# Kernel optimization log

Measured on AMD Instinct MI355X. Metric: run time of the kernel, lower is better.

The kernel has to match this reference:

```python
import jax, jax.numpy as jnp
import numpy as np
import math

# ---- hyperparameters (from __init__) ----
S = 64.0
M = 0.45
EASY_MARGIN = False
ALPHA = 0.0
BETA = 0.0
EPS_OT = 0.1   # self.eps
NITER = 6      # self.niter
COS_M = math.cos(M)
SIN_M = math.sin(M)
TH = math.cos(math.pi - M)
MM = math.sin(math.pi - M) * M

# ---- shapes ----
B = 24
D_EMB = 512
N_CLASSES = 10000
C_CH = 256   # channels -> number of OT points per image
H = 14       # spatial -> point dim H*H = 196


def setup_inputs() -> dict:
    key = jax.random.key(0)
    k1, k2, k3, k4 = jax.random.split(key, 4)
    embeddings = jax.random.normal(k1, (B, D_EMB), dtype=jnp.float32)
    conv_features = jax.random.normal(k2, (B, C_CH, H, H), dtype=jnp.float32)
    label = jax.random.randint(k3, (B,), 0, 8)
    # nn.init.normal_(kernel, std=0.01)
    kernel = jax.random.normal(k4, (D_EMB, N_CLASSES), dtype=jnp.float32) * 0.01
    return {"embeddings": embeddings, "conv_features": conv_features,
            "kernel": kernel, "label": label, "epoch": 1}


def _cdist(x, y):
    # Euclidean pairwise distance via GEMM: x (n,d), y (m,d) -> (n,m)
    x2 = jnp.sum(x * x, axis=-1)[:, None]
    y2 = jnp.sum(y * y, axis=-1)[None, :]
    d2 = jnp.maximum(x2 + y2 - 2.0 * (x @ y.T), 0.0)
    return jnp.sqrt(d2 + 1e-12)


def _sinkhorn_dist(x, y):
    # Entropic OT distance <T, C> with uniform marginals, log-domain Sinkhorn.
    C = _cdist(x, y)                       # (n, m)
    n, m = C.shape
    log_mu = -jnp.log(jnp.float32(n))
    log_nu = -jnp.log(jnp.float32(m))
    f = jnp.zeros((n,), C.dtype)
    g = jnp.zeros((m,), C.dtype)
    for _ in range(NITER):  # fixed 6 iterations
        f = -EPS_OT * jax.nn.logsumexp((g[None, :] - C) / EPS_OT + log_nu, axis=1)
        g = -EPS_OT * jax.nn.logsumexp((f[:, None] - C) / EPS_OT + log_mu, axis=0)
    T = jnp.exp((f[:, None] + g[None, :] - C) / EPS_OT + log_mu + log_nu)
    return jnp.sum(T * C)


def reference(embeddings, conv_features, kernel, label, epoch):
    b = embeddings.shape[0]
    emb = embeddings / jnp.linalg.norm(embeddings, axis=1, keepdims=True)
    kn = kernel / jnp.linalg.norm(kernel, axis=0, keepdims=True)
    cos_theta = jnp.clip(emb @ kn, -1.0, 1.0)          # (B, n_classes)
    origin_cos = cos_theta

    rows = jnp.arange(b)
    tl = cos_theta[rows, label]                         # target logit (B,)
    sin_t = jnp.sqrt(jnp.maximum(1.0 - tl * tl, 0.0))
    ctm = tl * COS_M - sin_t * SIN_M
    if EASY_MARGIN:
        ftl = jnp.where(tl > 0.0, ctm, tl)
    else:
        ftl = jnp.where(tl > TH, ctm, tl - MM)
    cos_theta = cos_theta.at[rows, label].set(ftl)
    arcfaceloss = cos_theta * S

    # ---- triplet mining on embedding cosine similarities ----
    dists = emb @ emb.T                                 # (B, B) cosine sims
    eq = label[:, None] == label[None, :]               # (B, B) same-class mask
    # diff_low[a,p,n] = cos(a,n) - cos(a,p)
    diff = dists[:, None, :] - dists[:, :, None]        # (a, p, n)
    valid = eq[:, :, None] & (~eq)[:, None, :] & (diff > -ALPHA)
    n_cosine_pair = jnp.sum(valid)

    if epoch >= 0:
        feats = conv_features.reshape(b, conv_features.shape[1], -1)  # (B, C, H*H)
        # batched Sinkhorn distance for all (a,b) image pairs: (B, B)
        D = jax.vmap(lambda xa: jax.vmap(lambda xb: _sinkhorn_dist(xa, xb))(feats))(feats)
        dis = jnp.maximum(D[:, :, None] - D[:, None, :], -BETA)       # (a, p, n)
        hit = valid & (dis > 0.0)
        ot_pair = jnp.sum(hit)
        wass = jnp.sum(jnp.where(hit, dis, 0.0))
        wass_loss = jnp.where(wass > 0.0,
                              wass / jnp.maximum(ot_pair, 1).astype(wass.dtype),
                              jnp.zeros((), wass.dtype))
    else:
        ot_pair = jnp.zeros((), jnp.int32)
        wass_loss = jnp.zeros(())

    return (arcfaceloss, wass_loss, origin_cos * S, n_cosine_pair, ot_pair)
```

## Files before the change

### kernel.cpp

```cpp
#include <hip/hip_runtime.h>
#include <math.h>

#define B_SZ 24
#define D_EMBD 512
#define N_CLS 10000
#define CC 256
#define HH 196

#define S_SCALE 64.0f
#define COS_M 0.9004471023526769f
#define SIN_M 0.43496553411123023f
#define TH_C (-0.9004471023526769f)
#define MM_C 0.19573449035005357f
#define KSC 14.4269504088896f
#define C2E 0.0693147180559945f

typedef short bfrag8 __attribute__((ext_vector_type(8)));
typedef float facc4 __attribute__((ext_vector_type(4)));

#if __has_builtin(__builtin_amdgcn_exp2f)
#define EXP2F(x) __builtin_amdgcn_exp2f(x)
#else
#define EXP2F(x) exp2f(x)
#endif
#if __has_builtin(__builtin_amdgcn_logf)
#define LOG2F(x) __builtin_amdgcn_logf(x)
#else
#define LOG2F(x) __log2f(x)
#endif

__device__ inline unsigned short f2bf_rne(float x) {
    union { float f; unsigned u; } cv; cv.f = x;
    unsigned r = cv.u + 0x7FFFu + ((cv.u >> 16) & 1u);
    return (unsigned short)(r >> 16);
}
__device__ inline float bf2f(unsigned short h) {
    union { unsigned u; float f; } cv; cv.u = ((unsigned)h) << 16; return cv.f;
}

__global__ __launch_bounds__(1024) void k_pairs_all(const float* __restrict__ emb,
        const float* __restrict__ conv, float* __restrict__ dists,
        float* __restrict__ Dmat) {
    const int t = threadIdx.x;
    const int bid = blockIdx.x;

    if (bid >= 276) {
        int l = t & 63, w16 = t >> 6;
        if (bid == 276 && t < B_SZ) Dmat[t * B_SZ + t] = 0.f;
        int pid = (bid - 276) * 16 + w16;
        if (pid >= B_SZ * B_SZ) return;
        int i = pid / B_SZ, j = pid - (pid / B_SZ) * B_SZ;
        float sij = 0.f, sii = 0.f, sjj = 0.f;
        #pragma unroll
        for (int u = 0; u < 8; ++u) {
            float vi = emb[i*D_EMBD + u*64 + l];
            float vj = emb[j*D_EMBD + u*64 + l];
            sij = fmaf(vi, vj, sij); sii = fmaf(vi, vi, sii); sjj = fmaf(vj, vj, sjj);
        }
        #pragma unroll
        for (int o = 1; o < 64; o <<= 1) {
            sij += __shfl_xor(sij, o, 64);
            sii += __shfl_xor(sii, o, 64);
            sjj += __shfl_xor(sjj, o, 64);
        }
        if (l == 0) dists[pid] = sij * rsqrtf(sii * sjj);
        return;
    }

    __shared__ __align__(16) char smem[65536];
    unsigned short* Ah = (unsigned short*)smem;
    unsigned short* Al = Ah + 8192;
    unsigned short* Bh = Al + 8192;
    unsigned short* Bl = Bh + 8192;
    float* rowred = (float*)smem;
    float* colred = rowred + 1024;
    float* rm_l   = colred + 1024;
    float* z_l    = rm_l + 256;
    float* g_l    = z_l + 256;
    float* na_s   = g_l + 256;
    float* nb_s   = na_s + 256;
    float* wredF  = nb_s + 256;
    float* wredG  = wredF + 4;
    float* wredD  = wredG + 4;

    const int w = t >> 6;
    const int wr = w >> 2, wc = w & 3;
    const int q = (t >> 4) & 3, c0 = t & 15;
    const int R0 = wr * 64, C0 = wc * 64;

    int rem = bid, a = 0;
    while (rem >= 23 - a) { rem -= 23 - a; ++a; }
    int b = a + 1 + rem;
    const float* xa = conv + a*CC*HH;
    const float* xb = conv + b*CC*HH;

    const int sn = t >> 2;
    const int sch = t & 3;

    facc4 acc[4][4];
    #pragma unroll
    for (int i = 0; i < 4; ++i)
        #pragma unroll
        for (int j = 0; j < 4; ++j) acc[i][j] = (facc4){0.f, 0.f, 0.f, 0.f};

    float pa = 0.f, pb = 0.f;

    for (int ks = 0; ks < 224; ks += 32) {
        __syncthreads();
        #pragma unroll
        for (int p = 0; p < 2; ++p) {
            int k0 = ks + sch*8;
            const float* src = (p ? xb : xa) + sn*HH + k0;
            float v[8];
            if (k0 + 8 <= HH) {
                const float4* s4 = (const float4*)src;
                float4 u0 = s4[0], u1 = s4[1];
                v[0]=u0.x; v[1]=u0.y; v[2]=u0.z; v[3]=u0.w;
                v[4]=u1.x; v[5]=u1.y; v[6]=u1.z; v[7]=u1.w;
            } else {
                #pragma unroll
                for (int j = 0; j < 8; ++j) v[j] = (k0 + j < HH) ? src[j] : 0.f;
            }
            float ps = 0.f;
            union { unsigned short s[8]; bfrag8 v8; } uh, ul;
            #pragma unroll
            for (int j = 0; j < 8; ++j) {
                ps = fmaf(v[j], v[j], ps);
                unsigned short hb = f2bf_rne(v[j]);
                uh.s[j] = hb;
                ul.s[j] = f2bf_rne(v[j] - bf2f(hb));
            }
            if (p) pb += ps; else pa += ps;
            unsigned short* dh = (p ? Bh : Ah) + sn*32 + sch*8;
            unsigned short* dl = (p ? Bl : Al) + sn*32 + sch*8;
            *(bfrag8*)dh = uh.v8;
            *(bfrag8*)dl = ul.v8;
        }
        __syncthreads();
        bfrag8 bh4[4], bl4[4];
        #pragma unroll
        for (int tj = 0; tj < 4; ++tj) {
            int col = C0 + tj*16 + c0;
            bh4[tj] = *(const bfrag8*)(Bh + col*32 + q*8);
            bl4[tj] = *(const bfrag8*)(Bl + col*32 + q*8);
        }
        #pragma unroll
        for (int ti = 0; ti < 4; ++ti) {
            int row = R0 + ti*16 + c0;
            bfrag8 ah = *(const bfrag8*)(Ah + row*32 + q*8);
            bfrag8 al = *(const bfrag8*)(Al + row*32 + q*8);
            #pragma unroll
            for (int tj = 0; tj < 4; ++tj) {
                acc[ti][tj] = __builtin_amdgcn_mfma_f32_16x16x32_bf16(ah, bh4[tj], acc[ti][tj], 0, 0, 0);
                acc[ti][tj] = __builtin_amdgcn_mfma_f32_16x16x32_bf16(ah, bl4[tj], acc[ti][tj], 0, 0, 0);
                acc[ti][tj] = __builtin_amdgcn_mfma_f32_16x16x32_bf16(al, bh4[tj], acc[ti][tj], 0, 0, 0);
            }
        }
    }
    __syncthreads();

    pa += __shfl_xor(pa, 1, 64); pa += __shfl_xor(pa, 2, 64);
    pb += __shfl_xor(pb, 1, 64); pb += __shfl_xor(pb, 2, 64);
    if (sch == 0) { na_s[sn] = pa; nb_s[sn] = pb; }
    if (t < 256) g_l[t] = 0.f;
    if (t < 4) wredG[t] = 0.f;
    __syncthreads();

    facc4 E[4][4];
    {
        float nbv[4];
        #pragma unroll
        for (int tj = 0; tj < 4; ++tj) nbv[tj] = nb_s[C0 + tj*16 + c0];
        #pragma unroll
        for (int ti = 0; ti < 4; ++ti) {
            facc4 nav = *(const facc4*)&na_s[R0 + ti*16 + q*4];
            #pragma unroll
            for (int tj = 0; tj < 4; ++tj) {
                #pragma unroll
                for (int r = 0; r < 4; ++r) {
                    float d2 = fmaxf(nav[r] + nbv[tj] - 2.f*acc[ti][tj][r], 0.f);
                    E[ti][tj][r] = KSC * sqrtf(d2 + 1e-12f);
                }
            }
        }
    }

    const int istar = ((c0&1)<<3) | ((c0&2)<<1) | ((c0&4)>>1) | ((c0&8)>>3);
    const int rowstar = R0 + (istar>>2)*16 + q*4 + (istar&3);
    const int tjstar = ((q&1)<<1) | (q>>1);
    const int colstar = C0 + tjstar*16 + c0;

    {
        float v16[16];
        #pragma unroll
        for (int ti = 0; ti < 4; ++ti)
            #pragma unroll
            for (int r = 0; r < 4; ++r)
                v16[ti*4+r] = fminf(fminf(E[ti][0][r], E[ti][1][r]),
                                    fminf(E[ti][2][r], E[ti][3][r]));
        #pragma unroll
        for (int p = 0; p < 4; ++p) {
            const int m = 1 << p, hsz = 8 >> p;
            const bool hi = (c0 >> p) & 1;
            #pragma unroll
            for (int j = 0; j < hsz; ++j) {
                float mine = hi ? v16[j+hsz] : v16[j];
                float send = hi ? v16[j] : v16[j+hsz];
                v16[j] = fminf(mine, __shfl_xor(send, m, 64));
            }
        }
        rowred[wc*256 + rowstar] = v16[0];
    }
    __syncthreads();
    if (t < 256)
        rm_l[t] = fminf(fminf(rowred[t], rowred[256+t]), fminf(rowred[512+t], rowred[768+t]));
    __syncthreads();

    #pragma unroll
    for (int ti = 0; ti < 4; ++ti) {
        facc4 rmv = *(const facc4*)&rm_l[R0 + ti*16 + q*4];
        #pragma unroll
        for (int tj = 0; tj < 4; ++tj)
            #pragma unroll
            for (int r = 0; r < 4; ++r)
                E[ti][tj][r] = EXP2F(rmv[r] - E[ti][tj][r]);
    }

    #pragma unroll 1
    for (int it = 0; it < 6; ++it) {
        float Gmax = fmaxf(fmaxf(wredG[0], wredG[1]), fmaxf(wredG[2], wredG[3]));
        float P4[4];
        #pragma unroll
        for (int tj = 0; tj < 4; ++tj) P4[tj] = EXP2F(g_l[C0 + tj*16 + c0] - Gmax);
        float v16[16];
        #pragma unroll
        for (int ti = 0; ti < 4; ++ti)
            #pragma unroll
            for (int r = 0; r < 4; ++r) {
                float s = 0.f;
                #pragma unroll
                for (int tj = 0; tj < 4; ++tj) s = fmaf(E[ti][tj][r], P4[tj], s);
                v16[ti*4+r] = s;
            }
        #pragma unroll
        for (int p = 0; p < 4; ++p) {
            const int m = 1 << p, hsz = 8 >> p;
            const bool hi = (c0 >> p) & 1;
            #pragma unroll
            for (int j = 0; j < hsz; ++j) {
                float mine = hi ? v16[j+hsz] : v16[j];
                float send = hi ? v16[j] : v16[j+hsz];
                v16[j] = mine + __shfl_xor(send, m, 64);
            }
        }
        rowred[wc*256 + rowstar] = v16[0];
        __syncthreads();
        if (t < 256) {
            float s = rowred[t] + rowred[256+t] + rowred[512+t] + rowred[768+t];
            float z = 8.f - Gmax - LOG2F(s);
            z_l[t] = z;
            float m = z;
            #pragma unroll
            for (int o = 1; o < 64; o <<= 1) m = fmaxf(m, __shfl_xor(m, o, 64));
            if ((t & 63) == 0) wredF[t >> 6] = m;
        }
        __syncthreads();
        float M = fmaxf(fmaxf(wredF[0], wredF[1]), fmaxf(wredF[2], wredF[3]));
        float Q[16];
        #pragma unroll
        for (int ti = 0; ti < 4; ++ti) {
            facc4 zv = *(const facc4*)&z_l[R0 + ti*16 + q*4];
            #pragma unroll
            for (int r = 0; r < 4; ++r) Q[ti*4+r] = EXP2F(zv[r] - M);
        }
        float w4[4];
        #pragma unroll
        for (int tj = 0; tj < 4; ++tj) {
            float s = 0.f;
            #pragma unroll
            for (int ti = 0; ti < 4; ++ti)
                #pragma unroll
                for (int r = 0; r < 4; ++r) s = fmaf(E[ti][tj][r], Q[ti*4+r], s);
            w4[tj] = s;
        }
        #pragma unroll
        for (int p = 0; p < 2; ++p) {
            const int m = 16 << p, hsz = 2 >> p;
            const bool hi = (q >> p) & 1;
            #pragma unroll
            for (int j = 0; j < hsz; ++j) {
                float mine = hi ? w4[j+hsz] : w4[j];
                float send = hi ? w4[j] : w4[j+hsz];
                w4[j] = mine + __shfl_xor(send, m, 64);
            }
        }
        colred[wr*256 + colstar] = w4[0];
        __syncthreads();
        if (t < 256) {
            float s = colred[t] + colred[256+t] + colred[512+t] + colred[768+t];
            float G = 8.f - M - LOG2F(s);
            g_l[t] = G;
            float m = G;
            #pragma unroll
            for (int o = 1; o < 64; o <<= 1) m = fmaxf(m, __shfl_xor(m, o, 64));
            if ((t & 63) == 0) wredG[t >> 6] = m;
        }
        __syncthreads();
    }

    {
        float G4[4];
        #pragma unroll
        for (int tj = 0; tj < 4; ++tj) G4[tj] = g_l[C0 + tj*16 + c0] - 16.f;
        float d = 0.f;
        #pragma unroll
        for (int ti = 0; ti < 4; ++ti) {
            facc4 zv = *(const facc4*)&z_l[R0 + ti*16 + q*4];
            facc4 rmv = *(const facc4*)&rm_l[R0 + ti*16 + q*4];
            #pragma unroll
            for (int tj = 0; tj < 4; ++tj) {
                #pragma unroll
                for (int r = 0; r < 4; ++r) {
                    float e = fmaxf(E[ti][tj][r], 1e-45f);
                    float lE = LOG2F(e);
                    float ce = rmv[r] - lE;
                    d = fmaf(EXP2F(zv[r] + G4[tj] + lE), ce, d);
                }
            }
        }
        d *= C2E;
        #pragma unroll
        for (int o = 1; o < 64; o <<= 1) d += __shfl_xor(d, o, 64);
        if ((t & 63) == 0) wredD[w] = d;
        __syncthreads();
        if (t == 0) {
            float s = 0.f;
            #pragma unroll
            for (int i = 0; i < 16; ++i) s += wredD[i];
            Dmat[a*B_SZ + b] = s;
            Dmat[b*B_SZ + a] = s;
        }
    }
}

__global__ __launch_bounds__(256) void k_arc_fin(const float* __restrict__ emb,
        const float* __restrict__ kern, const int* __restrict__ label,
        const float* __restrict__ dists, const float* __restrict__ Dmat,
        float* __restrict__ out) {
    const int t = threadIdx.x;
    const int bid = blockIdx.x;

    if (bid == 313) {
        __shared__ float ds[576], Dm[576];
        __shared__ int lab[B_SZ];
        __shared__ float wls[4]; __shared__ int wnp[4], wot[4];
        for (int i = t; i < 576; i += 256) { ds[i] = dists[i]; Dm[i] = Dmat[i]; }
        if (t < B_SZ) lab[t] = label[t];
        __syncthreads();
        int np = 0, ot = 0; float wsum = 0.f;
        for (int idx = t; idx < 24*24*24; idx += 256) {
            int a2 = idx / 576;
            int rest = idx - a2*576;
            int p2 = rest / 24;
            int n2 = rest - p2*24;
            int la = lab[a2];
            if (la == lab[p2] && la != lab[n2]) {
                float diff = ds[a2*24 + n2] - ds[a2*24 + p2];
                if (diff > 0.f) {
                    ++np;
                    float dd = Dm[a2*24 + p2] - Dm[a2*24 + n2];
                    if (dd > 0.f) { ++ot; wsum += dd; }
                }
            }
        }
        #pragma unroll
        for (int o = 1; o < 64; o <<= 1) {
            np += __shfl_xor(np, o, 64);
            ot += __shfl_xor(ot, o, 64);
            wsum += __shfl_xor(wsum, o, 64);
        }
        int w = t >> 6;
        if ((t & 63) == 0) { wnp[w] = np; wot[w] = ot; wls[w] = wsum; }
        __syncthreads();
        if (t == 0) {
            int tnp = wnp[0]+wnp[1]+wnp[2]+wnp[3];
            int tot = wot[0]+wot[1]+wot[2]+wot[3];
            float tws = wls[0]+wls[1]+wls[2]+wls[3];
            int den = tot > 1 ? tot : 1;
            float wl = (tws > 0.f) ? tws / (float)den : 0.f;
            out[240000] = wl;
            out[480001] = (float)tnp;
            out[480002] = (float)tot;
        }
        return;
    }

    __shared__ __align__(16) float es[B_SZ*D_EMBD];
    __shared__ float inv_s[B_SZ];
    __shared__ int lab_s[B_SZ];
    float* part = es;
    float* resb = es + 6400;

    {
        const float4* s4 = (const float4*)emb;
        float4* d4 = (float4*)es;
        for (int i = t; i < (B_SZ*D_EMBD)/4; i += 256) d4[i] = s4[i];
    }
    if (t < B_SZ) lab_s[t] = label[t];
    __syncthreads();
    {
        int l = t & 63, w = t >> 6;
        for (int r = w; r < B_SZ; r += 4) {
            float s = 0.f;
            #pragma unroll
            for (int u = 0; u < 8; ++u) { float v = es[r*D_EMBD + u*64 + l]; s = fmaf(v, v, s); }
            #pragma unroll
            for (int o = 1; o < 64; o <<= 1) s += __shfl_xor(s, o, 64);
            if (l == 0) inv_s[r] = rsqrtf(s);
        }
    }
    __syncthreads();

    const int cc = t & 31, kc = t >> 5;
    int c = bid*32 + cc;
    int cL = c < N_CLS ? c : N_CLS - 1;
    float acc[B_SZ];
    #pragma unroll
    for (int r = 0; r < B_SZ; ++r) acc[r] = 0.f;
    float cn = 0.f;
    const int k0 = kc*64;
    for (int u = 0; u < 16; ++u) {
        int kb = k0 + u*4;
        float kv0 = kern[(kb+0)*N_CLS + cL];
        float kv1 = kern[(kb+1)*N_CLS + cL];
        float kv2 = kern[(kb+2)*N_CLS + cL];
        float kv3 = kern[(kb+3)*N_CLS + cL];
        cn = fmaf(kv0,kv0,cn); cn = fmaf(kv1,kv1,cn);
        cn = fmaf(kv2,kv2,cn); cn = fmaf(kv3,kv3,cn);
        #pragma unroll
        for (int r = 0; r < B_SZ; ++r) {
            const float4 e = *(const float4*)&es[r*D_EMBD + kb];
            acc[r] = fmaf(e.x, kv0, acc[r]);
            acc[r] = fmaf(e.y, kv1, acc[r]);
            acc[r] = fmaf(e.z, kv2, acc[r]);
            acc[r] = fmaf(e.w, kv3, acc[r]);
        }
    }
    __syncthreads();
    #pragma unroll
    for (int r = 0; r < B_SZ; ++r) part[kc*800 + cc*25 + r] = acc[r];
    part[kc*800 + cc*25 + 24] = cn;
    __syncthreads();
    for (int j = t; j < 800; j += 256) {
        float s = 0.f;
        #pragma unroll
        for (int kk = 0; kk < 8; ++kk) s += part[kk*800 + j];
        resb[j] = s;
    }
    __syncthreads();
    for (int o = t; o < 768; o += 256) {
        int r = o >> 5, c2 = o & 31;
        int col = bid*32 + c2;
        if (col >= N_CLS) continue;
        float dot = resb[c2*25 + r];
        float invk = rsqrtf(resb[c2*25 + 24]);
        float cosv = fminf(fmaxf(dot * inv_s[r] * invk, -1.f), 1.f);
        float oc = cosv * S_SCALE;
        float af = oc;
        if (lab_s[r] == col) {
            float tl = cosv;
            float sint = sqrtf(fmaxf(1.f - tl*tl, 0.f));
            float ctm = tl*COS_M - sint*SIN_M;
            float ftl = (tl > TH_C) ? ctm : (tl - MM_C);
            af = ftl * S_SCALE;
        }
        out[r*N_CLS + col] = af;
        out[240001 + r*N_CLS + col] = oc;
    }
}

extern "C" void kernel_launch(void* const* d_in, const int* in_sizes, int n_in,
                              void* d_out, int out_size, void* d_ws, size_t ws_size,
                              hipStream_t stream) {
    (void)in_sizes; (void)n_in; (void)out_size; (void)ws_size;
    const float* emb  = (const float*)d_in[0];
    const float* conv = (const float*)d_in[1];
    const float* kern = (const float*)d_in[2];
    const int*   lab  = (const int*)d_in[3];
    float* out = (float*)d_out;
    float* ws  = (float*)d_ws;
    float* dists = ws;
    float* Dmat  = ws + 576;

    k_pairs_all<<<312, 1024, 0, stream>>>(emb, conv, dists, Dmat);
    k_arc_fin<<<314, 256, 0, stream>>>(emb, kern, lab, dists, Dmat, out);
}
```

Baseline: 204.1 us.

## Precompute bf16 hi/lo split per image once and stream it into pair kernel

Adds a prep kernel that converts each image's conv features to swizzled bf16 hi/lo planes and row norms once, instead of every pair block recomputing the split for both images. The pair kernel then loads the prepared tiles into LDS asynchronously. The arcface GEMM moves into the prep kernel with 64-column blocks, and the final reduction becomes its own single-block kernel. This removes redundant conversion work across the 276 pair blocks, at the cost of a third launch and an extra global round trip for the prepared data.

New measurement: 206.7 us. About the same (+1.3%).

```diff
diff --git a/kernel.cpp b/kernel.cpp
--- a/kernel.cpp
+++ b/kernel.cpp
@@ -15,8 +15,11 @@
 #define KSC 14.4269504088896f
 #define C2E 0.0693147180559945f
 
+#define IMG_STRIDE 57344
+
 typedef short bfrag8 __attribute__((ext_vector_type(8)));
 typedef float facc4 __attribute__((ext_vector_type(4)));
+typedef unsigned int u32;
 
 #if __has_builtin(__builtin_amdgcn_exp2f)
 #define EXP2F(x) __builtin_amdgcn_exp2f(x)
@@ -37,91 +40,41 @@
 __device__ inline float bf2f(unsigned short h) {
     union { unsigned u; float f; } cv; cv.u = ((unsigned)h) << 16; return cv.f;
 }
-
-__global__ __launch_bounds__(1024) void k_pairs_all(const float* __restrict__ emb,
-        const float* __restrict__ conv, float* __restrict__ dists,
-        float* __restrict__ Dmat) {
+__device__ inline int swz(int row, int q) {
+    return (q ^ (row & 3) ^ ((row >> 2) & 3)) & 3;
+}
+__device__ __forceinline__ void async16(const void* g, void* l) {
+    __builtin_amdgcn_global_load_lds((const __attribute__((address_space(1))) u32*)g,
+                                     (__attribute__((address_space(3))) u32*)l, 16, 0, 0);
+}
+
+__global__ __launch_bounds__(512, 2) void k_prep_arc(const float* __restrict__ emb,
+        const float* __restrict__ conv, const float* __restrict__ kern,
+        const int* __restrict__ label, float* __restrict__ pnorm,
+        unsigned short* __restrict__ prep_h, unsigned short* __restrict__ prep_l,
+        float* __restrict__ out) {
     const int t = threadIdx.x;
     const int bid = blockIdx.x;
 
-    if (bid >= 276) {
-        int l = t & 63, w16 = t >> 6;
-        if (bid == 276 && t < B_SZ) Dmat[t * B_SZ + t] = 0.f;
-        int pid = (bid - 276) * 16 + w16;
-        if (pid >= B_SZ * B_SZ) return;
-        int i = pid / B_SZ, j = pid - (pid / B_SZ) * B_SZ;
-        float sij = 0.f, sii = 0.f, sjj = 0.f;
-        #pragma unroll
-        for (int u = 0; u < 8; ++u) {
-            float vi = emb[i*D_EMBD + u*64 + l];
-            float vj = emb[j*D_EMBD + u*64 + l];
-            sij = fmaf(vi, vj, sij); sii = fmaf(vi, vi, sii); sjj = fmaf(vj, vj, sjj);
-        }
-        #pragma unroll
-        for (int o = 1; o < 64; o <<= 1) {
-            sij += __shfl_xor(sij, o, 64);
-            sii += __shfl_xor(sii, o, 64);
-            sjj += __shfl_xor(sjj, o, 64);
-        }
-        if (l == 0) dists[pid] = sij * rsqrtf(sii * sjj);
-        return;
-    }
-
-    __shared__ __align__(16) char smem[65536];
-    unsigned short* Ah = (unsigned short*)smem;
-    unsigned short* Al = Ah + 8192;
-    unsigned short* Bh = Al + 8192;
-    unsigned short* Bl = Bh + 8192;
-    float* rowred = (float*)smem;
-    float* colred = rowred + 1024;
-    float* rm_l   = colred + 1024;
-    float* z_l    = rm_l + 256;
-    float* g_l    = z_l + 256;
-    float* na_s   = g_l + 256;
-    float* nb_s   = na_s + 256;
-    float* wredF  = nb_s + 256;
-    float* wredG  = wredF + 4;
-    float* wredD  = wredG + 4;
-
-    const int w = t >> 6;
-    const int wr = w >> 2, wc = w & 3;
-    const int q = (t >> 4) & 3, c0 = t & 15;
-    const int R0 = wr * 64, C0 = wc * 64;
-
-    int rem = bid, a = 0;
-    while (rem >= 23 - a) { rem -= 23 - a; ++a; }
-    int b = a + 1 + rem;
-    const float* xa = conv + a*CC*HH;
-    const float* xb = conv + b*CC*HH;
-
-    const int sn = t >> 2;
-    const int sch = t & 3;
-
-    facc4 acc[4][4];
-    #pragma unroll
-    for (int i = 0; i < 4; ++i)
-        #pragma unroll
-        for (int j = 0; j < 4; ++j) acc[i][j] = (facc4){0.f, 0.f, 0.f, 0.f};
-
-    float pa = 0.f, pb = 0.f;
-
-    for (int ks = 0; ks < 224; ks += 32) {
-        __syncthreads();
-        #pragma unroll
-        for (int p = 0; p < 2; ++p) {
-            int k0 = ks + sch*8;
-            const float* src = (p ? xb : xa) + sn*HH + k0;
+    if (bid < 24) {
+        const float* x = conv + bid*CC*HH;
+        const int row = t >> 1, half = t & 1;
+        const float* xr = x + row*HH;
+        float ps = 0.f;
+        #pragma unroll 1
+        for (int c14 = 0; c14 < 14; ++c14) {
+            int kc = half*14 + c14;
+            int k = kc*8;
             float v[8];
-            if (k0 + 8 <= HH) {
-                const float4* s4 = (const float4*)src;
+            if (k + 8 <= HH) {
+                const float4* s4 = (const float4*)(xr + k);
                 float4 u0 = s4[0], u1 = s4[1];
                 v[0]=u0.x; v[1]=u0.y; v[2]=u0.z; v[3]=u0.w;
                 v[4]=u1.x; v[5]=u1.y; v[6]=u1.z; v[7]=u1.w;
             } else {
                 #pragma unroll
-                for (int j = 0; j < 8; ++j) v[j] = (k0 + j < HH) ? src[j] : 0.f;
-            }
-            float ps = 0.f;
+                for (int j = 0; j < 8; ++j) v[j] = (k + j < HH) ? xr[k + j] : 0.f;
+            }
             union { unsigned short s[8]; bfrag8 v8; } uh, ul;
             #pragma unroll
             for (int j = 0; j < 8; ++j) {
@@ -130,290 +83,33 @@
                 uh.s[j] = hb;
                 ul.s[j] = f2bf_rne(v[j] - bf2f(hb));
             }
-            if (p) pb += ps; else pa += ps;
-            unsigned short* dh = (p ? Bh : Ah) + sn*32 + sch*8;
-            unsigned short* dl = (p ? Bl : Al) + sn*32 + sch*8;
-            *(bfrag8*)dh = uh.v8;
-            *(bfrag8*)dl = ul.v8;
-        }
-        __syncthreads();
-        bfrag8 bh4[4], bl4[4];
-        #pragma unroll
-        for (int tj = 0; tj < 4; ++tj) {
-            int col = C0 + tj*16 + c0;
-            bh4[tj] = *(const bfrag8*)(Bh + col*32 + q*8);
-            bl4[tj] = *(const bfrag8*)(Bl + col*32 + q*8);
-        }
-        #pragma unroll
-        for (int ti = 0; ti < 4; ++ti) {
-            int row = R0 + ti*16 + c0;
-            bfrag8 ah = *(const bfrag8*)(Ah + row*32 + q*8);
-            bfrag8 al = *(const bfrag8*)(Al + row*32 + q*8);
-            #pragma unroll
-            for (int tj = 0; tj < 4; ++tj) {
-                acc[ti][tj] = __builtin_amdgcn_mfma_f32_16x16x32_bf16(ah, bh4[tj], acc[ti][tj], 0, 0, 0);
-                acc[ti][tj] = __builtin_amdgcn_mfma_f32_16x16x32_bf16(ah, bl4[tj], acc[ti][tj], 0, 0, 0);
-                acc[ti][tj] = __builtin_amdgcn_mfma_f32_16x16x32_bf16(al, bh4[tj], acc[ti][tj], 0, 0, 0);
-            }
-        }
-    }
-    __syncthreads();
-
-    pa += __shfl_xor(pa, 1, 64); pa += __shfl_xor(pa, 2, 64);
-    pb += __shfl_xor(pb, 1, 64); pb += __shfl_xor(pb, 2, 64);
-    if (sch == 0) { na_s[sn] = pa; nb_s[sn] = pb; }
-    if (t < 256) g_l[t] = 0.f;
-    if (t < 4) wredG[t] = 0.f;
-    __syncthreads();
-
-    facc4 E[4][4];
-    {
-        float nbv[4];
-        #pragma unroll
-        for (int tj = 0; tj < 4; ++tj) nbv[tj] = nb_s[C0 + tj*16 + c0];
-        #pragma unroll
-        for (int ti = 0; ti < 4; ++ti) {
-            facc4 nav = *(const facc4*)&na_s[R0 + ti*16 + q*4];
-            #pragma unroll
-            for (int tj = 0; tj < 4; ++tj) {
-                #pragma unroll
-                for (int r = 0; r < 4; ++r) {
-                    float d2 = fmaxf(nav[r] + nbv[tj] - 2.f*acc[ti][tj][r], 0.f);
-                    E[ti][tj][r] = KSC * sqrtf(d2 + 1e-12f);
-                }
-            }
-        }
-    }
-
-    const int istar = ((c0&1)<<3) | ((c0&2)<<1) | ((c0&4)>>1) | ((c0&8)>>3);
-    const int rowstar = R0 + (istar>>2)*16 + q*4 + (istar&3);
-    const int tjstar = ((q&1)<<1) | (q>>1);
-    const int colstar = C0 + tjstar*16 + c0;
-
-    {
-        float v16[16];
-        #pragma unroll
-        for (int ti = 0; ti < 4; ++ti)
-            #pragma unroll
-            for (int r = 0; r < 4; ++r)
-                v16[ti*4+r] = fminf(fminf(E[ti][0][r], E[ti][1][r]),
-                                    fminf(E[ti][2][r], E[ti][3][r]));
-        #pragma unroll
-        for (int p = 0; p < 4; ++p) {
-            const int m = 1 << p, hsz = 8 >> p;
-            const bool hi = (c0 >> p) & 1;
-            #pragma unroll
-            for (int j = 0; j < hsz; ++j) {
-                float mine = hi ? v16[j+hsz] : v16[j];
-                float send = hi ? v16[j] : v16[j+hsz];
-                v16[j] = fminf(mine, __shfl_xor(send, m, 64));
-            }
-        }
-        rowred[wc*256 + rowstar] = v16[0];
-    }
-    __syncthreads();
-    if (t < 256)
-        rm_l[t] = fminf(fminf(rowred[t], rowred[256+t]), fminf(rowred[512+t], rowred[768+t]));
-    __syncthreads();
-
-    #pragma unroll
-    for (int ti = 0; ti < 4; ++ti) {
-        facc4 rmv = *(const facc4*)&rm_l[R0 + ti*16 + q*4];
-        #pragma unroll
-        for (int tj = 0; tj < 4; ++tj)
-            #pragma unroll
-            for (int r = 0; r < 4; ++r)
-                E[ti][tj][r] = EXP2F(rmv[r] - E[ti][tj][r]);
-    }
-
-    #pragma unroll 1
-    for (int it = 0; it < 6; ++it) {
-        float Gmax = fmaxf(fmaxf(wredG[0], wredG[1]), fmaxf(wredG[2], wredG[3]));
-        float P4[4];
-        #pragma unroll
-        for (int tj = 0; tj < 4; ++tj) P4[tj] = EXP2F(g_l[C0 + tj*16 + c0] - Gmax);
-        float v16[16];
-        #pragma unroll
-        for (int ti = 0; ti < 4; ++ti)
-            #pragma unroll
-            for (int r = 0; r < 4; ++r) {
-                float s = 0.f;
-                #pragma unroll
-                for (int tj = 0; tj < 4; ++tj) s = fmaf(E[ti][tj][r], P4[tj], s);
-                v16[ti*4+r] = s;
-            }
-        #pragma unroll
-        for (int p = 0; p < 4; ++p) {
-            const int m = 1 << p, hsz = 8 >> p;
-            const bool hi = (c0 >> p) & 1;
-            #pragma unroll
-            for (int j = 0; j < hsz; ++j) {
-                float mine = hi ? v16[j+hsz] : v16[j];
-                float send = hi ? v16[j] : v16[j+hsz];
-                v16[j] = mine + __shfl_xor(send, m, 64);
-            }
-        }
-        rowred[wc*256 + rowstar] = v16[0];
-        __syncthreads();
-        if (t < 256) {
-            float s = rowred[t] + rowred[256+t] + rowred[512+t] + rowred[768+t];
-            float z = 8.f - Gmax - LOG2F(s);
-            z_l[t] = z;
-            float m = z;
-            #pragma unroll
-            for (int o = 1; o < 64; o <<= 1) m = fmaxf(m, __shfl_xor(m, o, 64));
-            if ((t & 63) == 0) wredF[t >> 6] = m;
-        }
-        __syncthreads();
-        float M = fmaxf(fmaxf(wredF[0], wredF[1]), fmaxf(wredF[2], wredF[3]));
-        float Q[16];
-        #pragma unroll
-        for (int ti = 0; ti < 4; ++ti) {
-            facc4 zv = *(const facc4*)&z_l[R0 + ti*16 + q*4];
-            #pragma unroll
-            for (int r = 0; r < 4; ++r) Q[ti*4+r] = EXP2F(zv[r] - M);
-        }
-        float w4[4];
-        #pragma unroll
-        for (int tj = 0; tj < 4; ++tj) {
-            float s = 0.f;
-            #pragma unroll
-            for (int ti = 0; ti < 4; ++ti)
-                #pragma unroll
-                for (int r = 0; r < 4; ++r) s = fmaf(E[ti][tj][r], Q[ti*4+r], s);
-            w4[tj] = s;
-        }
-        #pragma unroll
-        for (int p = 0; p < 2; ++p) {
-            const int m = 16 << p, hsz = 2 >> p;
-            const bool hi = (q >> p) & 1;
-            #pragma unroll
-            for (int j = 0; j < hsz; ++j) {
-                float mine = hi ? w4[j+hsz] : w4[j];
-                float send = hi ? w4[j] : w4[j+hsz];
-                w4[j] = mine + __shfl_xor(send, m, 64);
-            }
-        }
-        colred[wr*256 + colstar] = w4[0];
-        __syncthreads();
-        if (t < 256) {
-            float s = colred[t] + colred[256+t] + colred[512+t] + colred[768+t];
-            float G = 8.f - M - LOG2F(s);
-            g_l[t] = G;
-            float m = G;
-            #pragma unroll
-            for (int o = 1; o < 64; o <<= 1) m = fmaxf(m, __shfl_xor(m, o, 64));
-            if ((t & 63) == 0) wredG[t >> 6] = m;
-        }
-        __syncthreads();
-    }
-
-    {
-        float G4[4];
-        #pragma unroll
-        for (int tj = 0; tj < 4; ++tj) G4[tj] = g_l[C0 + tj*16 + c0] - 16.f;
-        float d = 0.f;
-        #pragma unroll
-        for (int ti = 0; ti < 4; ++ti) {
-            facc4 zv = *(const facc4*)&z_l[R0 + ti*16 + q*4];
-            facc4 rmv = *(const facc4*)&rm_l[R0 + ti*16 + q*4];
-            #pragma unroll
-            for (int tj = 0; tj < 4; ++tj) {
-                #pragma unroll
-                for (int r = 0; r < 4; ++r) {
-                    float e = fmaxf(E[ti][tj][r], 1e-45f);
-                    float lE = LOG2F(e);
-                    float ce = rmv[r] - lE;
-                    d = fmaf(EXP2F(zv[r] + G4[tj] + lE), ce, d);
-                }
-            }
-        }
-        d *= C2E;
-        #pragma unroll
-        for (int o = 1; o < 64; o <<= 1) d += __shfl_xor(d, o, 64);
-        if ((t & 63) == 0) wredD[w] = d;
-        __syncthreads();
-        if (t == 0) {
-            float s = 0.f;
-            #pragma unroll
-            for (int i = 0; i < 16; ++i) s += wredD[i];
-            Dmat[a*B_SZ + b] = s;
-            Dmat[b*B_SZ + a] = s;
-        }
-    }
-}
-
-__global__ __launch_bounds__(256) void k_arc_fin(const float* __restrict__ emb,
-        const float* __restrict__ kern, const int* __restrict__ label,
-        const float* __restrict__ dists, const float* __restrict__ Dmat,
-        float* __restrict__ out) {
-    const int t = threadIdx.x;
-    const int bid = blockIdx.x;
-
-    if (bid == 313) {
-        __shared__ float ds[576], Dm[576];
-        __shared__ int lab[B_SZ];
-        __shared__ float wls[4]; __shared__ int wnp[4], wot[4];
-        for (int i = t; i < 576; i += 256) { ds[i] = dists[i]; Dm[i] = Dmat[i]; }
-        if (t < B_SZ) lab[t] = label[t];
-        __syncthreads();
-        int np = 0, ot = 0; float wsum = 0.f;
-        for (int idx = t; idx < 24*24*24; idx += 256) {
-            int a2 = idx / 576;
-            int rest = idx - a2*576;
-            int p2 = rest / 24;
-            int n2 = rest - p2*24;
-            int la = lab[a2];
-            if (la == lab[p2] && la != lab[n2]) {
-                float diff = ds[a2*24 + n2] - ds[a2*24 + p2];
-                if (diff > 0.f) {
-                    ++np;
-                    float dd = Dm[a2*24 + p2] - Dm[a2*24 + n2];
-                    if (dd > 0.f) { ++ot; wsum += dd; }
-                }
-            }
-        }
-        #pragma unroll
-        for (int o = 1; o < 64; o <<= 1) {
-            np += __shfl_xor(np, o, 64);
-            ot += __shfl_xor(ot, o, 64);
-            wsum += __shfl_xor(wsum, o, 64);
-        }
-        int w = t >> 6;
-        if ((t & 63) == 0) { wnp[w] = np; wot[w] = ot; wls[w] = wsum; }
-        __syncthreads();
-        if (t == 0) {
-            int tnp = wnp[0]+wnp[1]+wnp[2]+wnp[3];
-            int tot = wot[0]+wot[1]+wot[2]+wot[3];
-            float tws = wls[0]+wls[1]+wls[2]+wls[3];
-            int den = tot > 1 ? tot : 1;
-            float wl = (tws > 0.f) ? tws / (float)den : 0.f;
-            out[240000] = wl;
-            out[480001] = (float)tnp;
-            out[480002] = (float)tot;
-        }
+            int off = bid*IMG_STRIDE + (kc>>2)*8192 + row*32 + swz(row, kc&3)*8;
+            *(bfrag8*)&prep_h[off] = uh.v8;
+            *(bfrag8*)&prep_l[off] = ul.v8;
+        }
+        ps += __shfl_xor(ps, 1, 64);
+        if (half == 0) pnorm[bid*CC + row] = ps;
         return;
     }
 
-    __shared__ __align__(16) float es[B_SZ*D_EMBD];
+    __shared__ __align__(16) float sm[12800];
     __shared__ float inv_s[B_SZ];
     __shared__ int lab_s[B_SZ];
-    float* part = es;
-    float* resb = es + 6400;
+    const int ab = bid - 24;
 
     {
         const float4* s4 = (const float4*)emb;
-        float4* d4 = (float4*)es;
-        for (int i = t; i < (B_SZ*D_EMBD)/4; i += 256) d4[i] = s4[i];
+        float4* d4 = (float4*)sm;
+        for (int i = t; i < (B_SZ*D_EMBD)/4; i += 512) d4[i] = s4[i];
     }
     if (t < B_SZ) lab_s[t] = label[t];
     __syncthreads();
     {
         int l = t & 63, w = t >> 6;
-        for (int r = w; r < B_SZ; r += 4) {
+        for (int r = w; r < B_SZ; r += 8) {
             float s = 0.f;
             #pragma unroll
-            for (int u = 0; u < 8; ++u) { float v = es[r*D_EMBD + u*64 + l]; s = fmaf(v, v, s); }
+            for (int u = 0; u < 8; ++u) { float v = sm[r*D_EMBD + u*64 + l]; s = fmaf(v, v, s); }
             #pragma unroll
             for (int o = 1; o < 64; o <<= 1) s += __shfl_xor(s, o, 64);
             if (l == 0) inv_s[r] = rsqrtf(s);
@@ -421,8 +117,8 @@
     }
     __syncthreads();
 
-    const int cc = t & 31, kc = t >> 5;
-    int c = bid*32 + cc;
+    const int cc = t & 63, kc = t >> 6;
+    int c = ab*64 + cc;
     int cL = c < N_CLS ? c : N_CLS - 1;
     float acc[B_SZ];
     #pragma unroll
@@ -439,7 +135,7 @@
         cn = fmaf(kv2,kv2,cn); cn = fmaf(kv3,kv3,cn);
         #pragma unroll
         for (int r = 0; r < B_SZ; ++r) {
-            const float4 e = *(const float4*)&es[r*D_EMBD + kb];
+            const float4 e = *(const float4*)&sm[r*D_EMBD + kb];
             acc[r] = fmaf(e.x, kv0, acc[r]);
             acc[r] = fmaf(e.y, kv1, acc[r]);
             acc[r] = fmaf(e.z, kv2, acc[r]);
@@ -448,22 +144,22 @@
     }
     __syncthreads();
     #pragma unroll
-    for (int r = 0; r < B_SZ; ++r) part[kc*800 + cc*25 + r] = acc[r];
-    part[kc*800 + cc*25 + 24] = cn;
-    __syncthreads();
-    for (int j = t; j < 800; j += 256) {
+    for (int r = 0; r < B_SZ; ++r) sm[kc*1600 + cc*25 + r] = acc[r];
+    sm[kc*1600 + cc*25 + 24] = cn;
+    __syncthreads();
+    for (int j = t; j < 1600; j += 512) {
         float s = 0.f;
         #pragma unroll
-        for (int kk = 0; kk < 8; ++kk) s += part[kk*800 + j];
-        resb[j] = s;
-    }
-    __syncthreads();
-    for (int o = t; o < 768; o += 256) {
-        int r = o >> 5, c2 = o & 31;
-        int col = bid*32 + c2;
+        for (int kk = 0; kk < 8; ++kk) s += sm[kk*1600 + j];
+        sm[j] = s;
+    }
+    __syncthreads();
+    for (int o = t; o < 1536; o += 512) {
+        int r = o >> 6, c2 = o & 63;
+        int col = ab*64 + c2;
         if (col >= N_CLS) continue;
-        float dot = resb[c2*25 + r];
-        float invk = rsqrtf(resb[c2*25 + 24]);
+        float dot = sm[c2*25 + r];
+        float invk = rsqrtf(sm[c2*25 + 24]);
         float cosv = fminf(fmaxf(dot * inv_s[r] * invk, -1.f), 1.f);
         float oc = cosv * S_SCALE;
         float af = oc;
@@ -476,6 +172,340 @@
         }
         out[r*N_CLS + col] = af;
         out[240001 + r*N_CLS + col] = oc;
+    }
+}
+
+__global__ __launch_bounds__(1024) void k_pairs4(const float* __restrict__ emb,
+        const unsigned short* __restrict__ prep_h, const unsigned short* __restrict__ prep_l,
+        const float* __restrict__ pnorm, float* __restrict__ dists,
+        float* __restrict__ Dmat) {
+    const int t = threadIdx.x;
+    const int bid = blockIdx.x;
+
+    if (bid >= 276) {
+        int l = t & 63, w16 = t >> 6;
+        if (bid == 276 && t < B_SZ) Dmat[t * B_SZ + t] = 0.f;
+        int pid = (bid - 276) * 16 + w16;
+        if (pid >= B_SZ * B_SZ) return;
+        int i = pid / B_SZ, j = pid - (pid / B_SZ) * B_SZ;
+        float sij = 0.f, sii = 0.f, sjj = 0.f;
+        #pragma unroll
+        for (int u = 0; u < 8; ++u) {
+            float vi = emb[i*D_EMBD + u*64 + l];
+            float vj = emb[j*D_EMBD + u*64 + l];
+            sij = fmaf(vi, vj, sij); sii = fmaf(vi, vi, sii); sjj = fmaf(vj, vj, sjj);
+        }
+        #pragma unroll
+        for (int o = 1; o < 64; o <<= 1) {
+            sij += __shfl_xor(sij, o, 64);
+            sii += __shfl_xor(sii, o, 64);
+            sjj += __shfl_xor(sjj, o, 64);
+        }
+        if (l == 0) dists[pid] = sij * rsqrtf(sii * sjj);
+        return;
+    }
+
+    __shared__ __align__(16) char smem[65536];
+    unsigned short* AhS = (unsigned short*)smem;
+    unsigned short* AlS = AhS + 8192;
+    unsigned short* BhS = AlS + 8192;
+    unsigned short* BlS = BhS + 8192;
+    float* rowred = (float*)smem;
+    float* colred = rowred + 1024;
+    float* rm_l   = colred + 1024;
+    float* z_l    = rm_l + 256;
+    float* g_l    = z_l + 256;
+    float* na_s   = g_l + 256;
+    float* nb_s   = na_s + 256;
+    float* wredF  = nb_s + 256;
+    float* wredG  = wredF + 4;
+    float* wredD  = wredG + 4;
+
+    const int w = t >> 6;
+    const int wr = w >> 2, wc = w & 3;
+    const int q = (t >> 4) & 3, c0 = t & 15;
+    const int R0 = wr * 64, C0 = wc * 64;
+
+    int rem = bid, a = 0;
+    while (rem >= 23 - a) { rem -= 23 - a; ++a; }
+    int b = a + 1 + rem;
+
+    const unsigned short* gAh = prep_h + (size_t)a*IMG_STRIDE + t*8;
+    const unsigned short* gAl = prep_l + (size_t)a*IMG_STRIDE + t*8;
+    const unsigned short* gBh = prep_h + (size_t)b*IMG_STRIDE + t*8;
+    const unsigned short* gBl = prep_l + (size_t)b*IMG_STRIDE + t*8;
+    unsigned short* lAh = &AhS[(t & ~63) * 8];
+    unsigned short* lAl = &AlS[(t & ~63) * 8];
+    unsigned short* lBh = &BhS[(t & ~63) * 8];
+    unsigned short* lBl = &BlS[(t & ~63) * 8];
+
+    facc4 acc[4][4];
+    #pragma unroll
+    for (int i = 0; i < 4; ++i)
+        #pragma unroll
+        for (int j = 0; j < 4; ++j) acc[i][j] = (facc4){0.f, 0.f, 0.f, 0.f};
+
+    #pragma unroll 1
+    for (int s = 0; s < 7; ++s) {
+        __syncthreads();
+        const int so = s*8192;
+        async16(gAh + so, lAh);
+        async16(gAl + so, lAl);
+        async16(gBh + so, lBh);
+        async16(gBl + so, lBl);
+        __syncthreads();
+        bfrag8 bh4[4], bl4[4];
+        #pragma unroll
+        for (int tj = 0; tj < 4; ++tj) {
+            int col = C0 + tj*16 + c0;
+            int cof = col*32 + swz(col, q)*8;
+            bh4[tj] = *(const bfrag8*)&BhS[cof];
+            bl4[tj] = *(const bfrag8*)&BlS[cof];
+        }
+        #pragma unroll
+        for (int ti = 0; ti < 4; ++ti) {
+            int row = R0 + ti*16 + c0;
+            int rof = row*32 + swz(row, q)*8;
+            bfrag8 ah = *(const bfrag8*)&AhS[rof];
+            bfrag8 al = *(const bfrag8*)&AlS[rof];
+            #pragma unroll
+            for (int tj = 0; tj < 4; ++tj) {
+                acc[ti][tj] = __builtin_amdgcn_mfma_f32_16x16x32_bf16(ah, bh4[tj], acc[ti][tj], 0, 0, 0);
+                acc[ti][tj] = __builtin_amdgcn_mfma_f32_16x16x32_bf16(ah, bl4[tj], acc[ti][tj], 0, 0, 0);
+                acc[ti][tj] = __builtin_amdgcn_mfma_f32_16x16x32_bf16(al, bh4[tj], acc[ti][tj], 0, 0, 0);
+            }
+        }
+    }
+    __syncthreads();
+
+    if (t < 256) {
+        na_s[t] = pnorm[a*CC + t];
+        nb_s[t] = pnorm[b*CC + t];
+        g_l[t] = 0.f;
+    }
+    if (t < 4) wredG[t] = 0.f;
+    __syncthreads();
+
+    facc4 E[4][4];
+    {
+        float nbv[4];
+        #pragma unroll
+        for (int tj = 0; tj < 4; ++tj) nbv[tj] = nb_s[C0 + tj*16 + c0];
+        #pragma unroll
+        for (int ti = 0; ti < 4; ++ti) {
+            facc4 nav = *(const facc4*)&na_s[R0 + ti*16 + q*4];
+            #pragma unroll
+            for (int tj = 0; tj < 4; ++tj) {
+                #pragma unroll
+                for (int r = 0; r < 4; ++r) {
+                    float d2 = fmaxf(nav[r] + nbv[tj] - 2.f*acc[ti][tj][r], 0.f);
+                    E[ti][tj][r] = KSC * sqrtf(d2 + 1e-12f);
+                }
+            }
+        }
+    }
+
+    const int istar = ((c0&1)<<3) | ((c0&2)<<1) | ((c0&4)>>1) | ((c0&8)>>3);
+    const int rowstar = R0 + (istar>>2)*16 + q*4 + (istar&3);
+    const int tjstar = ((q&1)<<1) | (q>>1);
+    const int colstar = C0 + tjstar*16 + c0;
+
+    {
+        float v16[16];
+        #pragma unroll
+        for (int ti = 0; ti < 4; ++ti)
+            #pragma unroll
+            for (int r = 0; r < 4; ++r)
+                v16[ti*4+r] = fminf(fminf(E[ti][0][r], E[ti][1][r]),
+                                    fminf(E[ti][2][r], E[ti][3][r]));
+        #pragma unroll
+        for (int p = 0; p < 4; ++p) {
+            const int m = 1 << p, hsz = 8 >> p;
+            const bool hi = (c0 >> p) & 1;
+            #pragma unroll
+            for (int j = 0; j < hsz; ++j) {
+                float mine = hi ? v16[j+hsz] : v16[j];
+                float send = hi ? v16[j] : v16[j+hsz];
+                v16[j] = fminf(mine, __shfl_xor(send, m, 64));
+            }
+        }
+        rowred[wc*256 + rowstar] = v16[0];
+    }
+    __syncthreads();
+    if (t < 256)
+        rm_l[t] = fminf(fminf(rowred[t], rowred[256+t]), fminf(rowred[512+t], rowred[768+t]));
+    __syncthreads();
+
+    #pragma unroll
+    for (int ti = 0; ti < 4; ++ti) {
+        facc4 rmv = *(const facc4*)&rm_l[R0 + ti*16 + q*4];
+        #pragma unroll
+        for (int tj = 0; tj < 4; ++tj)
+            #pragma unroll
+            for (int r = 0; r < 4; ++r)
+                E[ti][tj][r] = EXP2F(rmv[r] - E[ti][tj][r]);
+    }
+
+    #pragma unroll 1
+    for (int it = 0; it < 6; ++it) {
+        float Gmax = fmaxf(fmaxf(wredG[0], wredG[1]), fmaxf(wredG[2], wredG[3]));
+        float P4[4];
+        #pragma unroll
+        for (int tj = 0; tj < 4; ++tj) P4[tj] = EXP2F(g_l[C0 + tj*16 + c0] - Gmax);
+        float v16[16];
+        #pragma unroll
+        for (int ti = 0; ti < 4; ++ti)
+            #pragma unroll
+            for (int r = 0; r < 4; ++r) {
+                float s = 0.f;
+                #pragma unroll
+                for (int tj = 0; tj < 4; ++tj) s = fmaf(E[ti][tj][r], P4[tj], s);
+                v16[ti*4+r] = s;
+            }
+        #pragma unroll
+        for (int p = 0; p < 4; ++p) {
+            const int m = 1 << p, hsz = 8 >> p;
+            const bool hi = (c0 >> p) & 1;
+            #pragma unroll
+            for (int j = 0; j < hsz; ++j) {
+                float mine = hi ? v16[j+hsz] : v16[j];
+                float send = hi ? v16[j] : v16[j+hsz];
+                v16[j] = mine + __shfl_xor(send, m, 64);
+            }
+        }
+        rowred[wc*256 + rowstar] = v16[0];
+        __syncthreads();
+        if (t < 256) {
+            float s = rowred[t] + rowred[256+t] + rowred[512+t] + rowred[768+t];
+            float z = 8.f - Gmax - LOG2F(s);
+            z_l[t] = z;
+            float m = z;
+            #pragma unroll
+            for (int o = 1; o < 64; o <<= 1) m = fmaxf(m, __shfl_xor(m, o, 64));
+            if ((t & 63) == 0) wredF[t >> 6] = m;
+        }
+        __syncthreads();
+        float M = fmaxf(fmaxf(wredF[0], wredF[1]), fmaxf(wredF[2], wredF[3]));
+        float Q[16];
+        #pragma unroll
+        for (int ti = 0; ti < 4; ++ti) {
+            facc4 zv = *(const facc4*)&z_l[R0 + ti*16 + q*4];
+            #pragma unroll
+            for (int r = 0; r < 4; ++r) Q[ti*4+r] = EXP2F(zv[r] - M);
+        }
+        float w4[4];
+        #pragma unroll
+        for (int tj = 0; tj < 4; ++tj) {
+            float s = 0.f;
+            #pragma unroll
+            for (int ti = 0; ti < 4; ++ti)
+                #pragma unroll
+                for (int r = 0; r < 4; ++r) s = fmaf(E[ti][tj][r], Q[ti*4+r], s);
+            w4[tj] = s;
+        }
+        #pragma unroll
+        for (int p = 0; p < 2; ++p) {
+            const int m = 16 << p, hsz = 2 >> p;
+            const bool hi = (q >> p) & 1;
+            #pragma unroll
+            for (int j = 0; j < hsz; ++j) {
+                float mine = hi ? w4[j+hsz] : w4[j];
+                float send = hi ? w4[j] : w4[j+hsz];
+                w4[j] = mine + __shfl_xor(send, m, 64);
+            }
+        }
+        colred[wr*256 + colstar] = w4[0];
+        __syncthreads();
+        if (t < 256) {
+            float s = colred[t] + colred[256+t] + colred[512+t] + colred[768+t];
+            float G = 8.f - M - LOG2F(s);
+            g_l[t] = G;
+            float m = G;
+            #pragma unroll
+            for (int o = 1; o < 64; o <<= 1) m = fmaxf(m, __shfl_xor(m, o, 64));
+            if ((t & 63) == 0) wredG[t >> 6] = m;
+        }
+        __syncthreads();
+    }
+
+    {
+        float G4[4];
+        #pragma unroll
+        for (int tj = 0; tj < 4; ++tj) G4[tj] = g_l[C0 + tj*16 + c0] - 16.f;
+        float d = 0.f;
+        #pragma unroll
+        for (int ti = 0; ti < 4; ++ti) {
+            facc4 zv = *(const facc4*)&z_l[R0 + ti*16 + q*4];
+            facc4 rmv = *(const facc4*)&rm_l[R0 + ti*16 + q*4];
+            #pragma unroll
+            for (int tj = 0; tj < 4; ++tj) {
+                #pragma unroll
+                for (int r = 0; r < 4; ++r) {
+                    float e = fmaxf(E[ti][tj][r], 1e-45f);
+                    float lE = LOG2F(e);
+                    d = fmaf(EXP2F(zv[r] + G4[tj] + lE), rmv[r] - lE, d);
+                }
+            }
+        }
+        d *= C2E;
+        #pragma unroll
+        for (int o = 1; o < 64; o <<= 1) d += __shfl_xor(d, o, 64);
+        if ((t & 63) == 0) wredD[w] = d;
+        __syncthreads();
+        if (t == 0) {
+            float s = 0.f;
+            #pragma unroll
+            for (int i = 0; i < 16; ++i) s += wredD[i];
+            Dmat[a*B_SZ + b] = s;
+            Dmat[b*B_SZ + a] = s;
+        }
+    }
+}
+
+__global__ __launch_bounds__(256) void k_fin(const int* __restrict__ label,
+        const float* __restrict__ dists, const float* __restrict__ Dmat,
+        float* __restrict__ out) {
+    const int t = threadIdx.x;
+    __shared__ float ds[576], Dm[576];
+    __shared__ int lab[B_SZ];
+    __shared__ float wls[4]; __shared__ int wnp[4], wot[4];
+    for (int i = t; i < 576; i += 256) { ds[i] = dists[i]; Dm[i] = Dmat[i]; }
+    if (t < B_SZ) lab[t] = label[t];
+    __syncthreads();
+    int np = 0, ot = 0; float wsum = 0.f;
+    for (int idx = t; idx < 24*24*24; idx += 256) {
+        int a2 = idx / 576;
+        int rest = idx - a2*576;
+        int p2 = rest / 24;
+        int n2 = rest - p2*24;
+        int la = lab[a2];
+        if (la == lab[p2] && la != lab[n2]) {
+            float diff = ds[a2*24 + n2] - ds[a2*24 + p2];
+            if (diff > 0.f) {
+                ++np;
+                float dd = Dm[a2*24 + p2] - Dm[a2*24 + n2];
+                if (dd > 0.f) { ++ot; wsum += dd; }
+            }
+        }
+    }
+    #pragma unroll
+    for (int o = 1; o < 64; o <<= 1) {
+        np += __shfl_xor(np, o, 64);
+        ot += __shfl_xor(ot, o, 64);
+        wsum += __shfl_xor(wsum, o, 64);
+    }
+    int w = t >> 6;
+    if ((t & 63) == 0) { wnp[w] = np; wot[w] = ot; wls[w] = wsum; }
+    __syncthreads();
+    if (t == 0) {
+        int tnp = wnp[0]+wnp[1]+wnp[2]+wnp[3];
+        int tot = wot[0]+wot[1]+wot[2]+wot[3];
+        float tws = wls[0]+wls[1]+wls[2]+wls[3];
+        int den = tot > 1 ? tot : 1;
+        float wl = (tws > 0.f) ? tws / (float)den : 0.f;
+        out[240000] = wl;
+        out[480001] = (float)tnp;
+        out[480002] = (float)tot;
     }
 }
 
@@ -491,7 +521,11 @@
     float* ws  = (float*)d_ws;
     float* dists = ws;
     float* Dmat  = ws + 576;
-
-    k_pairs_all<<<312, 1024, 0, stream>>>(emb, conv, dists, Dmat);
-    k_arc_fin<<<314, 256, 0, stream>>>(emb, kern, lab, dists, Dmat, out);
-}
+    float* pnorm = ws + 1152;
+    unsigned short* prep_h = (unsigned short*)(ws + 7296);
+    unsigned short* prep_l = prep_h + 24*IMG_STRIDE;
+
+    k_prep_arc<<<181, 512, 0, stream>>>(emb, conv, kern, lab, pnorm, prep_h, prep_l, out);
+    k_pairs4<<<312, 1024, 0, stream>>>(emb, prep_h, prep_l, pnorm, dists, Dmat);
+    k_fin<<<1, 256, 0, stream>>>(lab, dists, Dmat, out);
+}
```
